# Optimization experiments

Hardware: AMD Instinct MI355X
Metric: run time of the kernel (lower is better)

## Reference

```python
import jax, jax.numpy as jnp
import numpy as np

B, CIN, COUT, H, W, K = 4, 64, 64, 128, 128, 3
KK = K * K


def setup_inputs() -> dict:
    key = jax.random.key(0)
    k = jax.random.split(key, 7)
    return {
        "input_feat": jax.random.normal(k[0], (B, CIN, H, W), jnp.float32),
        "inter": jax.random.normal(k[1], (B, CIN, H, W), jnp.float32),
        "fea": jax.random.normal(k[2], (B, 4 * CIN, 1, 1), jnp.float32),
        "weight": jax.random.uniform(k[3], (COUT, CIN, K, K), jnp.float32, -1.0, 1.0) / np.float32(np.sqrt(CIN * KK)),
        "bias": jnp.zeros((COUT,), jnp.float32),
        # conv_offset_mask params (torch zero-inits; small random values used so offsets/masks are non-trivial)
        "com_w": jax.random.normal(k[4], (3 * KK, CIN, K, K), jnp.float32) * 0.01,
        "com_b": jnp.zeros((3 * KK,), jnp.float32),
        "c1_w": jax.random.normal(k[5], (COUT, 4 * CIN), jnp.float32) / np.float32(np.sqrt(4 * CIN)),
        "c2_w": jax.random.normal(k[6], (COUT, COUT), jnp.float32) / np.float32(np.sqrt(COUT)),
    }


def reference(input_feat, inter, fea, weight, bias, com_w, com_b, c1_w, c2_w):
    b, c, h, w = input_feat.shape
    # offset/mask prediction: 3x3 conv, stride 1, pad 1 -> [b, 3*KK, h, w]
    om = jax.lax.conv_general_dilated(inter, com_w, (1, 1), ((1, 1), (1, 1)),
                                      dimension_numbers=("NCHW", "OIHW", "NCHW"))
    om = om + com_b[None, :, None, None]
    offset = jnp.concatenate([om[:, :KK], om[:, KK:2 * KK]], axis=1)  # [b, 2*KK, h, w]
    mask = jax.nn.sigmoid(om[:, 2 * KK:])                              # [b, KK, h, w]
    dy, dx = offset[:, 0::2], offset[:, 1::2]                          # mmcv interleaved (y, x) per tap

    # dynamic per-sample weight modulation (Cout == Cin, fea scales the in-channel axis)
    fvec = jnp.einsum('oc,bc->bo', c1_w, fea[:, :, 0, 0])              # [b, COUT]
    wdyn = weight[None] * fvec[:, None, :, None, None]                 # [b, COUT, CIN, K, K]

    # sampling coordinates: base grid (stride=1, pad=1, dil=1) + learned offsets
    ky = jnp.repeat(jnp.arange(K), K).astype(jnp.float32)              # [KK]
    kx = jnp.tile(jnp.arange(K), K).astype(jnp.float32)
    base_y = jnp.arange(h, dtype=jnp.float32)[None, :, None] - 1.0 + ky[:, None, None]  # [KK, h, 1]
    base_x = jnp.arange(w, dtype=jnp.float32)[None, None, :] - 1.0 + kx[:, None, None]  # [KK, 1, w]
    ys = base_y[None] + dy                                             # [b, KK, h, w]
    xs = base_x[None] + dx

    y0f = jnp.floor(ys); x0f = jnp.floor(xs)
    ly = ys - y0f; lx = xs - x0f
    y0 = y0f.astype(jnp.int32); x0 = x0f.astype(jnp.int32)
    xf = input_feat.reshape(b, c, h * w)

    def gather(yi, xi, wgt):
        valid = (yi >= 0) & (yi < h) & (xi >= 0) & (xi < w)
        idx = jnp.clip(yi, 0, h - 1) * w + jnp.clip(xi, 0, w - 1)      # [b, KK, h, w]
        v = jnp.take_along_axis(xf, idx.reshape(b, 1, -1), axis=2).reshape(b, c, KK, h, w)
        return v * (wgt * valid)[:, None]

    val = (gather(y0, x0, (1 - ly) * (1 - lx)) + gather(y0, x0 + 1, (1 - ly) * lx)
           + gather(y0 + 1, x0, ly * (1 - lx)) + gather(y0 + 1, x0 + 1, ly * lx))
    val = val * mask[:, None]                                          # modulated samples [b, c, KK, h, w]

    out = jnp.einsum('bocp,bcphw->bohw', wdyn.reshape(b, COUT, c, KK), val) + bias[None, :, None, None]
    return jnp.einsum('oc,bchw->bohw', c2_w, out)                      # c2: 1x1 conv, no bias
```

## Files before the change

kernel.cpp:

```cpp
#include <hip/hip_runtime.h>
#include <math.h>

#define BB 4
#define CIN 64
#define COUT 64
#define HH 128
#define WW 128
#define HW (HH*WW)

typedef __attribute__((ext_vector_type(8))) short short8;
typedef __attribute__((ext_vector_type(4))) float f32x4;
typedef __attribute__((ext_vector_type(4))) unsigned int uint4v;

static __device__ __forceinline__ unsigned short f2bf(float f) {
    unsigned int u = __builtin_bit_cast(unsigned int, f);
    u += 0x7fffu + ((u >> 16) & 1u);
    return (unsigned short)(u >> 16);
}
static __device__ __forceinline__ float bf2f(unsigned short h) {
    unsigned int u = ((unsigned int)h) << 16;
    return __builtin_bit_cast(float, u);
}

__global__ __launch_bounds__(256) void prep_kernel(
        const float* __restrict__ com_w, const float* __restrict__ c2w,
        const float* __restrict__ bias,
        unsigned short* __restrict__ wk2, float* __restrict__ bias2) {
    int id = blockIdx.x, tid = threadIdx.x;
    if (id < 80) {
        int i = id*256 + tid;
        int k = i & 31, oc = (i >> 5) & 31;
        int cc5 = i >> 10;
        int cg = cc5 / 5, ch = cc5 % 5;
        int tap = ch*2 + (k >> 4);
        int c = cg*16 + (k & 15);
        float v = 0.f;
        if (tap < 9 && oc < 27) v = com_w[((size_t)oc*64 + c)*9 + tap];
        wk2[i] = f2bf(v);
    } else if (tid < COUT) {
        float s2 = 0.f;
        for (int o = 0; o < COUT; ++o) s2 += c2w[tid*COUT + o] * bias[o];
        bias2[tid] = s2;
    }
}

static __device__ __forceinline__ void transpose_body(
        const float* __restrict__ srcb, unsigned short* __restrict__ dstb,
        int tb, int tid, float* lt ) {
    int b = tb >> 8;
    int px0 = (tb & 255) * 64;
    const float* src = srcb + (size_t)b*CIN*HW + px0;
    for (int i = tid; i < 4096; i += 256) {
        int c = i >> 6, px = i & 63;
        lt[c*65 + px] = src[(size_t)c*HW + px];
    }
    __syncthreads();
    int q = tid & 3, px = tid >> 2;
    unsigned short* dst = dstb + ((size_t)b*HW + px0 + px)*64 + q*16;
    #pragma unroll
    for (int s = 0; s < 2; ++s) {
        short8 pk;
        #pragma unroll
        for (int j = 0; j < 8; ++j)
            pk[j] = (short)f2bf(lt[(q*16 + s*8 + j)*65 + px]);
        *(short8*)(dst + s*8) = pk;
    }
}

static __device__ __forceinline__ void w2_body(
        int wid, int tid, const float* __restrict__ weight,
        const float* __restrict__ c2w, const float* __restrict__ c1w,
        const float* __restrict__ fea,
        unsigned short* __restrict__ w2b, float* c2s, float* wcol) {
    int o2 = tid & 63, ci = tid >> 6;
    int lane = tid & 63;
    int bp = wid >> 4;
    int c_base = (wid & 15)*4;
    int p = bp % 9, b = bp / 9;
    int c = c_base + ci;

    float part = 0.f;
    #pragma unroll
    for (int s = 0; s < 4; ++s)
        part += c1w[c*(4*CIN) + lane + s*64] * fea[b*(4*CIN) + lane + s*64];
    #pragma unroll
    for (int off = 32; off; off >>= 1) part += __shfl_down(part, off);
    float fv = __shfl(part, 0);

    for (int idx = tid; idx < 4096; idx += 256) {
        int o2r = idx >> 6, oc = idx & 63;
        c2s[oc*65 + o2r] = c2w[idx];
    }
    {
        int o = tid & 63, cw = tid >> 6;
        wcol[cw*64 + o] = weight[(o*CIN + (c_base + cw))*9 + p];
    }
    __syncthreads();
    float s = 0.f;
    #pragma unroll 8
    for (int o = 0; o < COUT; ++o) s += c2s[o*65 + o2] * wcol[ci*64 + o];
    w2b[(size_t)bp*4096 + o2*64 + c] = f2bf(s * fv);
}

static __device__ __forceinline__ void conv_lds_body(
        int id, int tid, const float* __restrict__ inter,
        const unsigned short* __restrict__ wk2, const float* __restrict__ com_b,
        float* __restrict__ om, float* smemf) {
    unsigned short* til = (unsigned short*)smemf;
    int b  = id >> 7;
    int t7 = id & 127;
    int by = t7 >> 3;
    int bx = t7 & 7;
    int x0 = bx*16, y0 = by*8;
    int lane = tid & 63, wv = tid >> 6;
    int nn = lane & 15, qq = lane >> 4;

    if (tid < 24) til[180*24 + tid] = 0;

    int scl = tid & 15, scc = tid >> 4;
    int sgx  = x0 + scc - 1;
    int sgxc = max(sgx, 0);
    float sfx = ((unsigned)sgx < WW) ? 1.f : 0.f;

    f32x4 acc[2][2];
    #pragma unroll
    for (int nt = 0; nt < 2; ++nt)
        #pragma unroll
        for (int mh = 0; mh < 2; ++mh)
            #pragma unroll
            for (int j = 0; j < 4; ++j) acc[nt][mh][j] = 0.f;

    for (int cg = 0; cg < 4; ++cg) {
        __syncthreads();
        const float* I = inter + ((size_t)(b*CIN + cg*16))*HW;

        {
            const float* colp = I + (size_t)scl*HW + sgxc;
            unsigned short* tp = til + scc*24 + scl;
            #pragma unroll
            for (int r = 0; r < 10; ++r) {
                int gy  = y0 + r - 1;
                int gyc = min(max(gy, 0), HH-1);
                float m = ((unsigned)gy < HH) ? sfx : 0.f;
                float v = colp[(size_t)gyc*WW] * m;
                tp[r*(18*24)] = f2bf(v);
            }
        }
        #pragma unroll
        for (int k = 0; k < 2; ++k) {
            int i = k*256 + tid;
            if (i < 320) {
                int cl  = i & 15;
                int ccb = (i >> 4) & 1;
                int r   = i >> 5;
                int gx  = x0 + 15 + ccb;
                int gy  = y0 + r - 1;
                int gxc = min(gx, WW-1);
                int gyc = min(max(gy, 0), HH-1);
                float m = (((unsigned)gy < HH) && ((unsigned)gx < WW)) ? 1.f : 0.f;
                float v = I[(size_t)cl*HW + gyc*WW + gxc] * m;
                til[(r*18 + 16 + ccb)*24 + cl] = f2bf(v);
            }
        }
        __syncthreads();

        #pragma unroll
        for (int ch = 0; ch < 5; ++ch) {
            short8 a0 = *(const short8*)(wk2 +
                (((size_t)(cg*5 + ch)*32 + nn)*32 + qq*8));
            short8 a1 = *(const short8*)(wk2 +
                (((size_t)(cg*5 + ch)*32 + 16 + nn)*32 + qq*8));
            int tap = ch*2 + (qq >> 1);
            #pragma unroll
            for (int nt = 0; nt < 2; ++nt) {
                int row = wv*2 + nt;
                int px_idx;
                if (tap > 8) px_idx = 180;
                else {
                    int ky = tap/3, kx = tap%3;
                    px_idx = (row + ky)*18 + (nn + kx);
                }
                short8 bfr = *(const short8*)(til + px_idx*24 + (qq&1)*8);
                acc[nt][0] = __builtin_amdgcn_mfma_f32_16x16x32_bf16(
                                 a0, bfr, acc[nt][0], 0, 0, 0);
                acc[nt][1] = __builtin_amdgcn_mfma_f32_16x16x32_bf16(
                                 a1, bfr, acc[nt][1], 0, 0, 0);
            }
        }
    }

    float* op = om + (size_t)b*27*HW;
    #pragma unroll
    for (int nt = 0; nt < 2; ++nt) {
        int pix = (y0 + wv*2 + nt)*WW + x0 + nn;
        #pragma unroll
        for (int mh = 0; mh < 2; ++mh)
            #pragma unroll
            for (int j = 0; j < 4; ++j) {
                int oc = mh*16 + qq*4 + j;
                if (oc < 27)
                    op[(size_t)oc*HW + pix] = acc[nt][mh][j] + com_b[oc];
            }
    }
}

__global__ __launch_bounds__(256) void main2_kernel(
        const float* __restrict__ input_feat,
        const float* __restrict__ inter,
        const unsigned short* __restrict__ wk2,
        const float* __restrict__ com_b,
        const float* __restrict__ weight,
        const float* __restrict__ c2w,
        const float* __restrict__ c1w,
        const float* __restrict__ fea,
        float* __restrict__ om, unsigned short* __restrict__ w2b,
        unsigned short* __restrict__ fT) {
    __shared__ __align__(16) float smem[4416];
    int id = blockIdx.x, tid = threadIdx.x;
    if (id < 512)        conv_lds_body(id, tid, inter, wk2, com_b, om, smem);
    else if (id < 1088)  w2_body(id - 512, tid, weight, c2w, c1w, fea, w2b,
                                 smem, smem + 64*65);
    else                 transpose_body(input_feat, fT, id - 1088, tid, smem);
}

__global__ __launch_bounds__(256) void dcn_main_kernel(
        const unsigned short* __restrict__ fT,
        const unsigned short* __restrict__ w2b,
        const float* __restrict__ bias2,
        const float* __restrict__ om,
        float* __restrict__ out) {
    __shared__ float red[16*2*64];
    int id = blockIdx.x;
    int xcd = id & 7;
    int jj  = id >> 3;
    int b   = xcd >> 1;
    int y   = jj & 127;
    int xq  = ((xcd & 1) << 1) | (jj >> 7);

    int t = threadIdx.x;
    int lane = t & 63, wv = t >> 6;
    int strip = wv >> 1, kh = wv & 1;
    int nn = lane & 15, qq = lane >> 4;
    int px0 = xq*32 + strip*16;
    int x = px0 + nn;
    int pix = y*WW + x;
    const unsigned short* Fb = fT + (size_t)b*HW*64;
    const float* omb = om + (size_t)b*27*HW;
    const unsigned short* w2p = w2b + (size_t)(b*9)*4096 + kh*32 + qq*8;
    int co = kh*32 + qq*8;

    f32x4 acc[4];
    #pragma unroll
    for (int mt = 0; mt < 4; ++mt)
        #pragma unroll
        for (int j = 0; j < 4; ++j)
            acc[mt][j] = kh ? bias2[mt*16 + qq*4 + j] : 0.f;

    float omy = omb[pix];
    float omx = omb[(size_t)HW + pix];
    float omm = omb[(size_t)18*HW + pix];

    #pragma unroll
    for (int p = 0; p < 9; ++p) {
        short8 afr[4];
        #pragma unroll
        for (int mt = 0; mt < 4; ++mt)
            afr[mt] = *(const short8*)(w2p + (size_t)p*4096 + (mt*16 + nn)*64);

        float mv = 1.f / (1.f + expf(-omm));
        float ysv = (float)(y - 1 + p/3) + omy;
        float xsv = (float)(x - 1 + p%3) + omx;
        float y0f = floorf(ysv), x0f = floorf(xsv);
        float ly = ysv - y0f, lx = xsv - x0f;
        int y0 = (int)y0f, x0i = (int)x0f;
        int y1 = y0 + 1, x1 = x0i + 1;
        float vy0 = (y0 >= 0 && y0 < HH) ? 1.f : 0.f;
        float vy1 = (y1 >= 0 && y1 < HH) ? 1.f : 0.f;
        float vx0 = (x0i >= 0 && x0i < WW) ? 1.f : 0.f;
        float vx1 = (x1 >= 0 && x1 < WW) ? 1.f : 0.f;
        float w00 = (1.f-ly)*(1.f-lx)*mv * vy0*vx0;
        float w01 = (1.f-ly)*lx      *mv * vy0*vx1;
        float w10 = ly      *(1.f-lx)*mv * vy1*vx0;
        float w11 = ly      *lx      *mv * vy1*vx1;
        int y0c = min(max(y0,0),HH-1), y1c = min(max(y1,0),HH-1);
        int x0c = min(max(x0i,0),WW-1), x1c = min(max(x1,0),WW-1);
        int i00 = y0c*WW + x0c, i01 = y0c*WW + x1c;
        int i10 = y1c*WW + x0c, i11 = y1c*WW + x1c;

        if (p < 8) {
            omy = omb[(size_t)(2*p+2)*HW + pix];
            omx = omb[(size_t)(2*p+3)*HW + pix];
            omm = omb[(size_t)(19+p )*HW + pix];
        }

        short8 c00 = *(const short8*)(Fb + (size_t)i00*64 + co);
        short8 c01 = *(const short8*)(Fb + (size_t)i01*64 + co);
        short8 c10 = *(const short8*)(Fb + (size_t)i10*64 + co);
        short8 c11 = *(const short8*)(Fb + (size_t)i11*64 + co);

        unsigned int pw[4];
        #pragma unroll
        for (int jp = 0; jp < 4; ++jp) {
            float v0 = w00*bf2f((unsigned short)c00[2*jp])
                     + w01*bf2f((unsigned short)c01[2*jp])
                     + w10*bf2f((unsigned short)c10[2*jp])
                     + w11*bf2f((unsigned short)c11[2*jp]);
            float v1 = w00*bf2f((unsigned short)c00[2*jp+1])
                     + w01*bf2f((unsigned short)c01[2*jp+1])
                     + w10*bf2f((unsigned short)c10[2*jp+1])
                     + w11*bf2f((unsigned short)c11[2*jp+1]);
            pw[jp] = (unsigned int)f2bf(v0) | ((unsigned int)f2bf(v1) << 16);
        }
        uint4v u4 = {pw[0], pw[1], pw[2], pw[3]};
        short8 bfr = __builtin_bit_cast(short8, u4);

        #pragma unroll
        for (int mt = 0; mt < 4; ++mt)
            acc[mt] = __builtin_amdgcn_mfma_f32_16x16x32_bf16(
                          afr[mt], bfr, acc[mt], 0, 0, 0);
    }

    if (kh == 0) {
        #pragma unroll
        for (int mt = 0; mt < 4; ++mt)
            #pragma unroll
            for (int j = 0; j < 4; ++j)
                red[(mt*4 + j)*128 + strip*64 + lane] = acc[mt][j];
    }
    __syncthreads();
    if (kh == 1) {
        float* outp = out + (size_t)b*COUT*HW + (size_t)y*WW + px0 + nn;
        #pragma unroll
        for (int mt = 0; mt < 4; ++mt)
            #pragma unroll
            for (int j = 0; j < 4; ++j)
                outp[(size_t)(mt*16 + qq*4 + j)*HW] =
                    acc[mt][j] + red[(mt*4 + j)*128 + strip*64 + lane];
    }
}

extern "C" void kernel_launch(void* const* d_in, const int* in_sizes, int n_in,
                              void* d_out, int out_size, void* d_ws, size_t ws_size,
                              hipStream_t stream) {
    const float* input_feat = (const float*)d_in[0];
    const float* inter      = (const float*)d_in[1];
    const float* fea        = (const float*)d_in[2];
    const float* weight     = (const float*)d_in[3];
    const float* bias       = (const float*)d_in[4];
    const float* com_w      = (const float*)d_in[5];
    const float* com_b      = (const float*)d_in[6];
    const float* c1w        = (const float*)d_in[7];
    const float* c2w        = (const float*)d_in[8];
    float* out = (float*)d_out;

    float* ws    = (float*)d_ws;
    float* bias2 = ws + 256;
    unsigned short* w2b = (unsigned short*)(ws + 512);
    float* om    = ws + 512 + 73728;
    unsigned short* wk2 = (unsigned short*)(om + 1769472);
    unsigned short* fT  = wk2 + 20480;

    prep_kernel<<<81, 256, 0, stream>>>(com_w, c2w, bias, wk2, bias2);
    main2_kernel<<<2112, 256, 0, stream>>>(input_feat, inter, wk2, com_b,
                                           weight, c2w, c1w, fea, om, w2b, fT);
    dcn_main_kernel<<<2048, 256, 0, stream>>>(fT, w2b, bias2, om, out);
}
```

Before: 177.6 us.

## Stage a 6x36 input neighborhood tile in LDS for bilinear gathers

Before the tap loop, each block cooperatively loads a 6-row by 36-column, 64-channel bf16 neighborhood of the transposed input into XOR-swizzled shared memory. Bilinear corner reads use this tile when all four corners fall inside it, and fall back to global gathers otherwise. The goal is to turn the many scattered global gathers into LDS reads that reuse data across pixels and taps. The cost is an up-front tile load plus a barrier, extra branching, and the shared buffer being reused for the reduction, which needs an extra sync.

```diff
diff --git a/kernel.cpp b/kernel.cpp
--- a/kernel.cpp
+++ b/kernel.cpp
@@ -229,7 +229,7 @@
         const float* __restrict__ bias2,
         const float* __restrict__ om,
         float* __restrict__ out) {
-    __shared__ float red[16*2*64];
+    __shared__ __align__(16) unsigned short gtile[6*36*64];
     int id = blockIdx.x;
     int xcd = id & 7;
     int jj  = id >> 3;
@@ -247,7 +247,27 @@
     const unsigned short* Fb = fT + (size_t)b*HW*64;
     const float* omb = om + (size_t)b*27*HW;
     const unsigned short* w2p = w2b + (size_t)(b*9)*4096 + kh*32 + qq*8;
-    int co = kh*32 + qq*8;
+    int co  = kh*32 + qq*8;
+    int cob = kh*64 + qq*16;
+
+    int ybase = min(max(y - 2, 0), HH - 6);
+    int xbase = min(max(xq*32 - 2, 0), WW - 36);
+
+    char* gt = (char*)gtile;
+    #pragma unroll
+    for (int it = 0; it < 7; ++it) {
+        int c = it*256 + t;
+        if (c < 1728) {
+            int pl = c >> 3;
+            int ci = c & 7;
+            int sy = (pl*1821) >> 16;
+            int sx = pl - sy*36;
+            short8 v = *(const short8*)(Fb +
+                ((size_t)(ybase + sy)*WW + xbase + sx)*64 + ci*8);
+            int bo = (pl*128 + ci*16) ^ ((pl & 7) << 4);
+            *(short8*)(gt + bo) = v;
+        }
+    }
 
     f32x4 acc[4];
     #pragma unroll
@@ -259,6 +279,7 @@
     float omy = omb[pix];
     float omx = omb[(size_t)HW + pix];
     float omm = omb[(size_t)18*HW + pix];
+    __syncthreads();
 
     #pragma unroll
     for (int p = 0; p < 9; ++p) {
@@ -284,8 +305,6 @@
         float w11 = ly      *lx      *mv * vy1*vx1;
         int y0c = min(max(y0,0),HH-1), y1c = min(max(y1,0),HH-1);
         int x0c = min(max(x0i,0),WW-1), x1c = min(max(x1,0),WW-1);
-        int i00 = y0c*WW + x0c, i01 = y0c*WW + x1c;
-        int i10 = y1c*WW + x0c, i11 = y1c*WW + x1c;
 
         if (p < 8) {
             omy = omb[(size_t)(2*p+2)*HW + pix];
@@ -293,10 +312,28 @@
             omm = omb[(size_t)(19+p )*HW + pix];
         }
 
-        short8 c00 = *(const short8*)(Fb + (size_t)i00*64 + co);
-        short8 c01 = *(const short8*)(Fb + (size_t)i01*64 + co);
-        short8 c10 = *(const short8*)(Fb + (size_t)i10*64 + co);
-        short8 c11 = *(const short8*)(Fb + (size_t)i11*64 + co);
+        short8 c00, c01, c10, c11;
+        {
+            int sy0 = y0c - ybase, sy1 = y1c - ybase;
+            int sx0 = x0c - xbase, sx1 = x1c - xbase;
+            bool allin = ((unsigned)sy0 < 6) & ((unsigned)sy1 < 6) &
+                         ((unsigned)sx0 < 36) & ((unsigned)sx1 < 36);
+            if (allin) {
+                int p00 = sy0*36 + sx0, p01 = sy0*36 + sx1;
+                int p10 = sy1*36 + sx0, p11 = sy1*36 + sx1;
+                c00 = *(const short8*)(gt + ((p00*128 + cob) ^ ((p00&7)<<4)));
+                c01 = *(const short8*)(gt + ((p01*128 + cob) ^ ((p01&7)<<4)));
+                c10 = *(const short8*)(gt + ((p10*128 + cob) ^ ((p10&7)<<4)));
+                c11 = *(const short8*)(gt + ((p11*128 + cob) ^ ((p11&7)<<4)));
+            } else {
+                int i00 = y0c*WW + x0c, i01 = y0c*WW + x1c;
+                int i10 = y1c*WW + x0c, i11 = y1c*WW + x1c;
+                c00 = *(const short8*)(Fb + (size_t)i00*64 + co);
+                c01 = *(const short8*)(Fb + (size_t)i01*64 + co);
+                c10 = *(const short8*)(Fb + (size_t)i10*64 + co);
+                c11 = *(const short8*)(Fb + (size_t)i11*64 + co);
+            }
+        }
 
         unsigned int pw[4];
         #pragma unroll
@@ -320,6 +357,8 @@
                           afr[mt], bfr, acc[mt], 0, 0, 0);
     }
 
+    __syncthreads();
+    float* red = (float*)gtile;
     if (kh == 0) {
         #pragma unroll
         for (int mt = 0; mt < 4; ++mt)
```

After: 161.9 us. 8.8% less time.

## Drop K-split reduction in DCN main kernel; each wave covers all channels

Applied to the files above, without the earlier changes.

Each wave now handles both channel halves of its 16-pixel strip instead of splitting input channels across two waves. This removes the LDS reduction and __syncthreads, and computes bilinear sampling coordinates and weights once per pixel instead of twice. Bilinear interpolation is also rewritten with packed f32x2 math and the v_cvt_pk_bf16_f32 instruction in place of manual rounding. The grid is halved to 1024 blocks, so each wave does more serial work and holds more registers, which lowers available parallelism and may reduce occupancy.

```diff
diff --git a/kernel.cpp b/kernel.cpp
--- a/kernel.cpp
+++ b/kernel.cpp
@@ -10,6 +10,7 @@
 
 typedef __attribute__((ext_vector_type(8))) short short8;
 typedef __attribute__((ext_vector_type(4))) float f32x4;
+typedef __attribute__((ext_vector_type(2))) float f32x2;
 typedef __attribute__((ext_vector_type(4))) unsigned int uint4v;
 
 static __device__ __forceinline__ unsigned short f2bf(float f) {
@@ -20,6 +21,17 @@
 static __device__ __forceinline__ float bf2f(unsigned short h) {
     unsigned int u = ((unsigned int)h) << 16;
     return __builtin_bit_cast(float, u);
+}
+static __device__ __forceinline__ unsigned int cvtpk_bf16(float lo, float hi) {
+    unsigned int r;
+    asm("v_cvt_pk_bf16_f32 %0, %1, %2" : "=v"(r) : "v"(lo), "v"(hi));
+    return r;
+}
+static __device__ __forceinline__ f32x2 bfpair(unsigned int u) {
+    f32x2 r;
+    r[0] = __builtin_bit_cast(float, u << 16);
+    r[1] = __builtin_bit_cast(float, u & 0xffff0000u);
+    return r;
 }
 
 __global__ __launch_bounds__(256) void prep_kernel(
@@ -229,32 +241,29 @@
         const float* __restrict__ bias2,
         const float* __restrict__ om,
         float* __restrict__ out) {
-    __shared__ float red[16*2*64];
     int id = blockIdx.x;
     int xcd = id & 7;
-    int jj  = id >> 3;
     int b   = xcd >> 1;
-    int y   = jj & 127;
-    int xq  = ((xcd & 1) << 1) | (jj >> 7);
+    int xh  = xcd & 1;
+    int y   = id >> 3;
 
     int t = threadIdx.x;
     int lane = t & 63, wv = t >> 6;
-    int strip = wv >> 1, kh = wv & 1;
     int nn = lane & 15, qq = lane >> 4;
-    int px0 = xq*32 + strip*16;
+    int px0 = xh*64 + wv*16;
     int x = px0 + nn;
     int pix = y*WW + x;
     const unsigned short* Fb = fT + (size_t)b*HW*64;
     const float* omb = om + (size_t)b*27*HW;
-    const unsigned short* w2p = w2b + (size_t)(b*9)*4096 + kh*32 + qq*8;
-    int co = kh*32 + qq*8;
+    const unsigned short* w2p = w2b + (size_t)(b*9)*4096 + qq*8;
+    int co = qq*8;
 
     f32x4 acc[4];
     #pragma unroll
     for (int mt = 0; mt < 4; ++mt)
         #pragma unroll
         for (int j = 0; j < 4; ++j)
-            acc[mt][j] = kh ? bias2[mt*16 + qq*4 + j] : 0.f;
+            acc[mt][j] = bias2[mt*16 + qq*4 + j];
 
     float omy = omb[pix];
     float omx = omb[(size_t)HW + pix];
@@ -262,10 +271,13 @@
 
     #pragma unroll
     for (int p = 0; p < 9; ++p) {
-        short8 afr[4];
-        #pragma unroll
-        for (int mt = 0; mt < 4; ++mt)
-            afr[mt] = *(const short8*)(w2p + (size_t)p*4096 + (mt*16 + nn)*64);
+        short8 afrL[4], afrH[4];
+        #pragma unroll
+        for (int mt = 0; mt < 4; ++mt) {
+            const unsigned short* ap = w2p + (size_t)p*4096 + (mt*16 + nn)*64;
+            afrL[mt] = *(const short8*)(ap);
+            afrH[mt] = *(const short8*)(ap + 32);
+        }
 
         float mv = 1.f / (1.f + expf(-omm));
         float ysv = (float)(y - 1 + p/3) + omy;
@@ -293,50 +305,67 @@
             omm = omb[(size_t)(19+p )*HW + pix];
         }
 
-        short8 c00 = *(const short8*)(Fb + (size_t)i00*64 + co);
-        short8 c01 = *(const short8*)(Fb + (size_t)i01*64 + co);
-        short8 c10 = *(const short8*)(Fb + (size_t)i10*64 + co);
-        short8 c11 = *(const short8*)(Fb + (size_t)i11*64 + co);
-
+        const unsigned short* p00 = Fb + (size_t)i00*64 + co;
+        const unsigned short* p01 = Fb + (size_t)i01*64 + co;
+        const unsigned short* p10 = Fb + (size_t)i10*64 + co;
+        const unsigned short* p11 = Fb + (size_t)i11*64 + co;
+        short8 c00L = *(const short8*)(p00);
+        short8 c01L = *(const short8*)(p01);
+        short8 c10L = *(const short8*)(p10);
+        short8 c11L = *(const short8*)(p11);
+        short8 c00H = *(const short8*)(p00 + 32);
+        short8 c01H = *(const short8*)(p01 + 32);
+        short8 c10H = *(const short8*)(p10 + 32);
+        short8 c11H = *(const short8*)(p11 + 32);
+
+        uint4v u00 = __builtin_bit_cast(uint4v, c00L);
+        uint4v u01 = __builtin_bit_cast(uint4v, c01L);
+        uint4v u10 = __builtin_bit_cast(uint4v, c10L);
+        uint4v u11 = __builtin_bit_cast(uint4v, c11L);
         unsigned int pw[4];
         #pragma unroll
         for (int jp = 0; jp < 4; ++jp) {
-            float v0 = w00*bf2f((unsigned short)c00[2*jp])
-                     + w01*bf2f((unsigned short)c01[2*jp])
-                     + w10*bf2f((unsigned short)c10[2*jp])
-                     + w11*bf2f((unsigned short)c11[2*jp]);
-            float v1 = w00*bf2f((unsigned short)c00[2*jp+1])
-                     + w01*bf2f((unsigned short)c01[2*jp+1])
-                     + w10*bf2f((unsigned short)c10[2*jp+1])
-                     + w11*bf2f((unsigned short)c11[2*jp+1]);
-            pw[jp] = (unsigned int)f2bf(v0) | ((unsigned int)f2bf(v1) << 16);
-        }
-        uint4v u4 = {pw[0], pw[1], pw[2], pw[3]};
-        short8 bfr = __builtin_bit_cast(short8, u4);
-
+            f32x2 A = bfpair(u00[jp]);
+            f32x2 B = bfpair(u01[jp]);
+            f32x2 C = bfpair(u10[jp]);
+            f32x2 D = bfpair(u11[jp]);
+            f32x2 r = A*w00 + B*w01 + C*w10 + D*w11;
+            pw[jp] = cvtpk_bf16(r[0], r[1]);
+        }
+        uint4v u4L = {pw[0], pw[1], pw[2], pw[3]};
+        short8 bfrL = __builtin_bit_cast(short8, u4L);
         #pragma unroll
         for (int mt = 0; mt < 4; ++mt)
             acc[mt] = __builtin_amdgcn_mfma_f32_16x16x32_bf16(
-                          afr[mt], bfr, acc[mt], 0, 0, 0);
-    }
-
-    if (kh == 0) {
+                          afrL[mt], bfrL, acc[mt], 0, 0, 0);
+
+        u00 = __builtin_bit_cast(uint4v, c00H);
+        u01 = __builtin_bit_cast(uint4v, c01H);
+        u10 = __builtin_bit_cast(uint4v, c10H);
+        u11 = __builtin_bit_cast(uint4v, c11H);
+        #pragma unroll
+        for (int jp = 0; jp < 4; ++jp) {
+            f32x2 A = bfpair(u00[jp]);
+            f32x2 B = bfpair(u01[jp]);
+            f32x2 C = bfpair(u10[jp]);
+            f32x2 D = bfpair(u11[jp]);
+            f32x2 r = A*w00 + B*w01 + C*w10 + D*w11;
+            pw[jp] = cvtpk_bf16(r[0], r[1]);
+        }
+        uint4v u4H = {pw[0], pw[1], pw[2], pw[3]};
+        short8 bfrH = __builtin_bit_cast(short8, u4H);
         #pragma unroll
         for (int mt = 0; mt < 4; ++mt)
-            #pragma unroll
-            for (int j = 0; j < 4; ++j)
-                red[(mt*4 + j)*128 + strip*64 + lane] = acc[mt][j];
-    }
-    __syncthreads();
-    if (kh == 1) {
-        float* outp = out + (size_t)b*COUT*HW + (size_t)y*WW + px0 + nn;
-        #pragma unroll
-        for (int mt = 0; mt < 4; ++mt)
-            #pragma unroll
-            for (int j = 0; j < 4; ++j)
-                outp[(size_t)(mt*16 + qq*4 + j)*HW] =
-                    acc[mt][j] + red[(mt*4 + j)*128 + strip*64 + lane];
-    }
+            acc[mt] = __builtin_amdgcn_mfma_f32_16x16x32_bf16(
+                          afrH[mt], bfrH, acc[mt], 0, 0, 0);
+    }
+
+    float* outp = out + (size_t)b*COUT*HW + (size_t)y*WW + px0 + nn;
+    #pragma unroll
+    for (int mt = 0; mt < 4; ++mt)
+        #pragma unroll
+        for (int j = 0; j < 4; ++j)
+            outp[(size_t)(mt*16 + qq*4 + j)*HW] = acc[mt][j];
 }
 
 extern "C" void kernel_launch(void* const* d_in, const int* in_sizes, int n_in,
@@ -363,5 +392,5 @@
     prep_kernel<<<81, 256, 0, stream>>>(com_w, c2w, bias, wk2, bias2);
     main2_kernel<<<2112, 256, 0, stream>>>(input_feat, inter, wk2, com_b,
                                            weight, c2w, c1w, fea, om, w2b, fT);
-    dcn_main_kernel<<<2048, 256, 0, stream>>>(fT, w2b, bias2, om, out);
-}
+    dcn_main_kernel<<<1024, 256, 0, stream>>>(fT, w2b, bias2, om, out);
+}
```

Result: no change. 177.8 us (+0.1%).
